# Performance work log

Hardware: AMD Instinct MI355X
Metric: run time of the kernel (lower is better)

Reference implementation:

```python
import jax, jax.numpy as jnp
import numpy as np

N_NODES = 50000
N_EDGES = 800000
IN_DIM = 256
HIDDEN = 64
HEADS1 = 4
HEADS2 = 1
N_CLASSES = 64
NEG_SLOPE = 0.2


def setup_inputs() -> dict:
    key = jax.random.key(0)
    ks = jax.random.split(key, 12)
    x = jax.random.normal(ks[0], (N_NODES, IN_DIM), dtype=jnp.float32)
    src = jax.random.randint(ks[1], (N_EDGES,), 0, N_NODES, dtype=jnp.int32)
    dst = jax.random.randint(ks[2], (N_EDGES,), 0, N_NODES, dtype=jnp.int32)
    s1 = 1.0 / np.sqrt(IN_DIM)
    s2 = 1.0 / np.sqrt(HIDDEN * HEADS1)
    W1 = jax.random.normal(ks[3], (IN_DIM, HEADS1 * HIDDEN), dtype=jnp.float32) * s1
    aL1 = jax.random.normal(ks[4], (HEADS1, HIDDEN), dtype=jnp.float32) * 0.1
    aR1 = jax.random.normal(ks[5], (HEADS1, HIDDEN), dtype=jnp.float32) * 0.1
    b1 = jnp.zeros((HEADS1 * HIDDEN,), dtype=jnp.float32)
    W2 = jax.random.normal(ks[6], (HEADS1 * HIDDEN, HEADS2 * N_CLASSES), dtype=jnp.float32) * s2
    aL2 = jax.random.normal(ks[7], (HEADS2, N_CLASSES), dtype=jnp.float32) * 0.1
    aR2 = jax.random.normal(ks[8], (HEADS2, N_CLASSES), dtype=jnp.float32) * 0.1
    b2 = jnp.zeros((HEADS2 * N_CLASSES,), dtype=jnp.float32)
    resW2 = jax.random.normal(ks[9], (HEADS1 * HIDDEN, HEADS2 * N_CLASSES), dtype=jnp.float32) * s2
    return {"x": x, "W1": W1, "aL1": aL1, "aR1": aR1, "b1": b1,
            "W2": W2, "aL2": aL2, "aR2": aR2, "b2": b2, "resW2": resW2,
            "src": src, "dst": dst}


def _gat_layer(h, W, aL, aR, b, src, dst, heads, out_dim, res_W=None, activation=None):
    n = h.shape[0]
    feat = (h @ W).reshape(n, heads, out_dim)          # [N, H, D]
    el = jnp.sum(feat * aL, axis=-1)                    # [N, H]
    er = jnp.sum(feat * aR, axis=-1)                    # [N, H]
    e = el[src] + er[dst]                               # [E, H]
    e = jnp.where(e > 0, e, NEG_SLOPE * e)              # leaky_relu
    # edge softmax over incoming edges of each destination node
    m = jax.ops.segment_max(e, dst, num_segments=n)
    ex = jnp.exp(e - m[dst])
    s = jax.ops.segment_sum(ex, dst, num_segments=n)
    sd = s[dst]
    a = ex / jnp.where(sd > 0, sd, 1.0)                 # [E, H]
    msg = feat[src] * a[:, :, None]                     # [E, H, D]
    rst = jax.ops.segment_sum(msg, dst, num_segments=n)  # [N, H, D]
    if res_W is not None:
        rst = rst + (h @ res_W).reshape(n, heads, out_dim)
    rst = rst + b.reshape(1, heads, out_dim)
    if activation is not None:
        rst = activation(rst)
    return rst


def reference(x, W1, aL1, aR1, b1, W2, aL2, aR2, b2, resW2, src, dst):
    h = _gat_layer(x, W1, aL1, aR1, b1, src, dst, HEADS1, HIDDEN,
                   res_W=None, activation=jax.nn.elu)
    h = h.reshape(N_NODES, HEADS1 * HIDDEN)             # flatten(1)
    h = _gat_layer(h, W2, aL2, aR2, b2, src, dst, HEADS2, N_CLASSES,
                   res_W=resW2, activation=None)
    return h.mean(axis=1)                               # mean over heads
```

## Files before the change

kernel.cpp:

```cpp
#include <hip/hip_runtime.h>
#include <hip/hip_bf16.h>
#include <math.h>

#define N_NODES 50000
#define N_EDGES 800000
#define IN_DIM  256
#define HID     64
#define H1      4
#define F1      256
#define NC      64
#define CHUNK   128
#define NB_SCAN 49
#define GEMM1_BLOCKS 800
#define FILL_BLOCKS  ((N_EDGES+255)/256)
#define HIST4_BLOCKS ((N_EDGES/4+255)/256)

typedef __attribute__((ext_vector_type(8))) short short8v;
typedef __attribute__((ext_vector_type(4))) float float4v;

__device__ __forceinline__ float bf2f(unsigned short u){
  union { unsigned int i; float f; } c; c.i = ((unsigned int)u) << 16; return c.f;
}


__global__ __launch_bounds__(256) void hist_prepw_kernel(
    const int* __restrict__ dst, int* __restrict__ counts,
    const float* __restrict__ W1, const float* __restrict__ W2,
    const float* __restrict__ resW2,
    __hip_bfloat16* __restrict__ W1T, __hip_bfloat16* __restrict__ B2T){
  int b = blockIdx.x;
  if (b < HIST4_BLOCKS){
    int e4 = b*256 + threadIdx.x;
    if (e4 < N_EDGES/4){
      int4 d = ((const int4*)dst)[e4];
      atomicAdd(&counts[d.x], 1);
      atomicAdd(&counts[d.y], 1);
      atomicAdd(&counts[d.z], 1);
      atomicAdd(&counts[d.w], 1);
    }
  } else {
    int i = (b - HIST4_BLOCKS)*256 + threadIdx.x;
    if (i < 256*256){
      int n = i >> 8, k = i & 255;
      W1T[n*256 + k] = __float2bfloat16(W1[k*256 + n]);
    } else if (i < 256*256 + 128*256){
      int j = i - 256*256;
      int n = j >> 8, k = j & 255;
      float v = (n < 64) ? W2[k*64 + n] : resW2[k*64 + (n - 64)];
      B2T[n*256 + k] = __float2bfloat16(v);
    }
  }
}


__global__ __launch_bounds__(1024) void scan1_kernel(const int* __restrict__ counts,
                                                     int* __restrict__ part,
                                                     int* __restrict__ bsum, int n){
  __shared__ int wsum[16];
  int b = blockIdx.x, tid = threadIdx.x;
  int i = b*1024 + tid;
  int lane = tid & 63, wid = tid >> 6;
  int x = (i < n) ? counts[i] : 0;
  #pragma unroll
  for (int off = 1; off < 64; off <<= 1){ int t = __shfl_up(x, off); if (lane >= off) x += t; }
  if (lane == 63) wsum[wid] = x;
  __syncthreads();
  if (wid == 0 && lane < 16){
    int w = wsum[lane];
    #pragma unroll
    for (int off = 1; off < 16; off <<= 1){ int t = __shfl_up(w, off); if (lane >= off) w += t; }
    wsum[lane] = w;
  }
  __syncthreads();
  int incl = x + (wid ? wsum[wid-1] : 0);
  if (i < n) part[i] = incl;
  if (tid == 1023) bsum[b] = incl;
}

__global__ __launch_bounds__(1024) void scan3_kernel(const int* __restrict__ part,
                                                     const int* __restrict__ bsum,
                                                     int* __restrict__ row_ptr,
                                                     int* __restrict__ cursor, int n){
  __shared__ int off_s;
  int b = blockIdx.x, tid = threadIdx.x;
  if (tid < 64){
    int orig = (tid < NB_SCAN) ? bsum[tid] : 0;
    int x = orig;
    #pragma unroll
    for (int o = 1; o < 64; o <<= 1){ int t = __shfl_up(x, o); if (tid >= o) x += t; }
    if (tid == b) off_s = x - orig;
  }
  __syncthreads();
  int i = b*1024 + tid;
  if (i < n){
    int v = part[i] + off_s;
    row_ptr[i+1] = v; cursor[i+1] = v;
  }
  if (i == 0){ row_ptr[0] = 0; cursor[0] = 0; }
}


template<int LAYER, bool AFP32>
__device__ __forceinline__ void gemm_body(
    const void* __restrict__ Araw,
    const __hip_bfloat16* __restrict__ BT,
    __hip_bfloat16* __restrict__ Fb,
    float* __restrict__ Res,
    float* __restrict__ el, float* __restrict__ er,
    const float* __restrict__ aL, const float* __restrict__ aR,
    int M, int bm, int bn)
{
  constexpr int K = 256;
  __shared__ __hip_bfloat16 As[128*72];
  __shared__ __hip_bfloat16 Bs[128*72];
  int tid = threadIdx.x;
  int lane = tid & 63, w = tid >> 6;
  int wr = w >> 1, wc = w & 1;
  int l15 = lane & 15, l4 = lane >> 4;

  float4v acc[4][4];
  #pragma unroll
  for (int i=0;i<4;i++)
    #pragma unroll
    for (int j=0;j<4;j++) acc[i][j] = (float4v){0.f,0.f,0.f,0.f};

  for (int kt = 0; kt < K; kt += 64){
    #pragma unroll
    for (int it = 0; it < 4; it++){
      int chunk = tid + it*256;
      int r = chunk >> 3, kc = (chunk & 7)*8;
      int arow = bm*128 + r;
      if (AFP32){
        const float* Af = (const float*)Araw;
        float4 v0 = make_float4(0,0,0,0), v1 = make_float4(0,0,0,0);
        if (arow < M){
          v0 = *(const float4*)&Af[(size_t)arow*K + kt + kc];
          v1 = *(const float4*)&Af[(size_t)arow*K + kt + kc + 4];
        }
        __hip_bfloat16 t[8] = {__float2bfloat16(v0.x),__float2bfloat16(v0.y),
                               __float2bfloat16(v0.z),__float2bfloat16(v0.w),
                               __float2bfloat16(v1.x),__float2bfloat16(v1.y),
                               __float2bfloat16(v1.z),__float2bfloat16(v1.w)};
        *(int4*)&As[r*72 + kc] = *(int4*)t;
      } else {
        const __hip_bfloat16* Ab = (const __hip_bfloat16*)Araw;
        int4 va = make_int4(0,0,0,0);
        if (arow < M) va = *(const int4*)&Ab[(size_t)arow*K + kt + kc];
        *(int4*)&As[r*72 + kc] = va;
      }
      int brow = bn*128 + r;
      int4 vb = *(const int4*)&BT[(size_t)brow*K + kt + kc];
      *(int4*)&Bs[r*72 + kc] = vb;
    }
    __syncthreads();
    short8v af[4][2], bfr[4][2];
    #pragma unroll
    for (int mi=0;mi<4;mi++)
      #pragma unroll
      for (int kf=0;kf<2;kf++)
        af[mi][kf] = *(const short8v*)&As[(wr*64 + mi*16 + l15)*72 + kf*32 + l4*8];
    #pragma unroll
    for (int ni=0;ni<4;ni++)
      #pragma unroll
      for (int kf=0;kf<2;kf++)
        bfr[ni][kf] = *(const short8v*)&Bs[(wc*64 + ni*16 + l15)*72 + kf*32 + l4*8];
    #pragma unroll
    for (int mi=0;mi<4;mi++)
      #pragma unroll
      for (int ni=0;ni<4;ni++){
        acc[mi][ni] = __builtin_amdgcn_mfma_f32_16x16x32_bf16(bfr[ni][0], af[mi][0], acc[mi][ni], 0,0,0);
        acc[mi][ni] = __builtin_amdgcn_mfma_f32_16x16x32_bf16(bfr[ni][1], af[mi][1], acc[mi][ni], 0,0,0);
      }
    __syncthreads();
  }

  if (LAYER == 1){
    int h = bn*2 + wc;
    float aLv[4][4], aRv[4][4];
    #pragma unroll
    for (int ni=0;ni<4;ni++){
      float4 a = *(const float4*)&aL[h*64 + ni*16 + l4*4];
      float4 bvv = *(const float4*)&aR[h*64 + ni*16 + l4*4];
      aLv[ni][0]=a.x; aLv[ni][1]=a.y; aLv[ni][2]=a.z; aLv[ni][3]=a.w;
      aRv[ni][0]=bvv.x; aRv[ni][1]=bvv.y; aRv[ni][2]=bvv.z; aRv[ni][3]=bvv.w;
    }
    #pragma unroll
    for (int mi=0;mi<4;mi++){
      int row = bm*128 + wr*64 + mi*16 + l15;
      float sl = 0.f, sr = 0.f;
      ushort4 packs[4];
      #pragma unroll
      for (int ni=0;ni<4;ni++){
        __hip_bfloat16 o[4];
        #pragma unroll
        for (int r=0;r<4;r++){
          float v = acc[mi][ni][r];
          sl += v*aLv[ni][r]; sr += v*aRv[ni][r];
          o[r] = __float2bfloat16(v);
        }
        packs[ni] = *(ushort4*)o;
      }
      if (row < M){
        #pragma unroll
        for (int ni=0;ni<4;ni++)
          *(ushort4*)&Fb[(size_t)row*256 + h*64 + ni*16 + l4*4] = packs[ni];
      }
      sl += __shfl_xor(sl, 16); sl += __shfl_xor(sl, 32);
      sr += __shfl_xor(sr, 16); sr += __shfl_xor(sr, 32);
      if (l4 == 0 && row < M){ el[row*4 + h] = sl; er[row*4 + h] = sr; }
    }
  } else {
    if (wc == 0){
      float aLv[4][4], aRv[4][4];
      #pragma unroll
      for (int ni=0;ni<4;ni++){
        float4 a = *(const float4*)&aL[ni*16 + l4*4];
        float4 bvv = *(const float4*)&aR[ni*16 + l4*4];
        aLv[ni][0]=a.x; aLv[ni][1]=a.y; aLv[ni][2]=a.z; aLv[ni][3]=a.w;
        aRv[ni][0]=bvv.x; aRv[ni][1]=bvv.y; aRv[ni][2]=bvv.z; aRv[ni][3]=bvv.w;
      }
      #pragma unroll
      for (int mi=0;mi<4;mi++){
        int row = bm*128 + wr*64 + mi*16 + l15;
        float sl = 0.f, sr = 0.f;
        ushort4 packs[4];
        #pragma unroll
        for (int ni=0;ni<4;ni++){
          __hip_bfloat16 o[4];
          #pragma unroll
          for (int r=0;r<4;r++){
            float v = acc[mi][ni][r];
            sl += v*aLv[ni][r]; sr += v*aRv[ni][r];
            o[r] = __float2bfloat16(v);
          }
          packs[ni] = *(ushort4*)o;
        }
        if (row < M){
          #pragma unroll
          for (int ni=0;ni<4;ni++)
            *(ushort4*)&Fb[(size_t)row*64 + ni*16 + l4*4] = packs[ni];
        }
        sl += __shfl_xor(sl, 16); sl += __shfl_xor(sl, 32);
        sr += __shfl_xor(sr, 16); sr += __shfl_xor(sr, 32);
        if (l4 == 0 && row < M){ el[row] = sl; er[row] = sr; }
      }
    } else {
      #pragma unroll
      for (int mi=0;mi<4;mi++){
        int row = bm*128 + wr*64 + mi*16 + l15;
        if (row < M){
          #pragma unroll
          for (int ni=0;ni<4;ni++){
            float4 o = make_float4(acc[mi][ni][0], acc[mi][ni][1], acc[mi][ni][2], acc[mi][ni][3]);
            *(float4*)&Res[(size_t)row*64 + ni*16 + l4*4] = o;
          }
        }
      }
    }
  }
}

__global__ __launch_bounds__(256) void gemm1_fill_kernel(
    const float* __restrict__ x, const __hip_bfloat16* __restrict__ W1T,
    __hip_bfloat16* __restrict__ featb,
    float* __restrict__ el, float* __restrict__ er,
    const float* __restrict__ aL, const float* __restrict__ aR,
    const int* __restrict__ src, const int* __restrict__ dst,
    int* __restrict__ cursor, int* __restrict__ csr_src)
{
  int id = blockIdx.x;
  if (id < GEMM1_BLOCKS){
    int bn = (id >> 3) & 1;
    int bm = (id & 7) | ((id >> 4) << 3);
    if (bm*128 >= N_NODES) return;
    gemm_body<1,true>(x, W1T, featb, nullptr, el, er, aL, aR, N_NODES, bm, bn);
  } else {
    int e = (id - GEMM1_BLOCKS)*256 + threadIdx.x;
    if (e < N_EDGES){
      int slot = atomicAdd(&cursor[dst[e]], 1);
      csr_src[slot] = src[e];
    }
  }
}

__global__ __launch_bounds__(256) void gemm2_kernel(
    const __hip_bfloat16* __restrict__ A, const __hip_bfloat16* __restrict__ BT,
    __hip_bfloat16* __restrict__ Fb, float* __restrict__ Res,
    float* __restrict__ el, float* __restrict__ er,
    const float* __restrict__ aL, const float* __restrict__ aR, int M)
{
  gemm_body<2,false>(A, BT, Fb, Res, el, er, aL, aR, M, blockIdx.x, 0);
}


__global__ __launch_bounds__(256) void agg1_kernel(const int* __restrict__ row_ptr,
                                                   const int* __restrict__ csr_src,
                                                   const float* __restrict__ el,
                                                   const float* __restrict__ er,
                                                   const __hip_bfloat16* __restrict__ featb,
                                                   const float* __restrict__ bias,
                                                   __hip_bfloat16* __restrict__ h1b, int N){
  __shared__ int   ssh[4][CHUNK];
  __shared__ float wsh[4][CHUNK][4];
  int b = blockIdx.x;
  int slot = b & 7, ch = slot >> 2, sub = slot & 3, g = b >> 3;
  int lane = threadIdx.x & 63, wv = threadIdx.x >> 6;
  int n = g*16 + sub*4 + wv;
  if (n >= N) return;
  int rs = row_ptr[n], re = row_ptr[n+1];
  int half = lane >> 5;
  int l31 = lane & 31;
  int c0 = ch*128 + l31*4;
  int hl = c0 >> 6;
  float4 ern4 = *(const float4*)&er[(size_t)n*4];
  float ernv[4] = {ern4.x, ern4.y, ern4.z, ern4.w};
  float acc[4] = {0.f,0.f,0.f,0.f};
  float ssum4[4] = {0.f,0.f,0.f,0.f};

  for (int base = rs; base < re; base += CHUNK){
    int cnt = min(CHUNK, re - base);
    int padded = (cnt + 7) & ~7;
    for (int t = lane; t < padded; t += 64){
      float w4[4] = {0.f,0.f,0.f,0.f};
      int s = 0;
      if (t < cnt){
        s = csr_src[base + t];
        float4 e4 = *(const float4*)&el[(size_t)s*4];
        float ev[4] = {e4.x, e4.y, e4.z, e4.w};
        #pragma unroll
        for (int h = 0; h < 4; h++){
          float e = ev[h] + ernv[h];
          e = e > 0.f ? e : 0.2f*e;
          float ex = __expf(e);
          w4[h] = ex;
          ssum4[h] += ex;
        }
      }
      ssh[wv][t] = s;
      *(float4*)&wsh[wv][t][0] = make_float4(w4[0], w4[1], w4[2], w4[3]);
    }
    for (int jb = 0; jb < padded; jb += 8){
      int t0 = jb + half, t1 = jb + 2 + half, t2 = jb + 4 + half, t3 = jb + 6 + half;
      int s0 = ssh[wv][t0], s1 = ssh[wv][t1], s2 = ssh[wv][t2], s3 = ssh[wv][t3];
      float w0 = wsh[wv][t0][hl], w1 = wsh[wv][t1][hl];
      float w2 = wsh[wv][t2][hl], w3 = wsh[wv][t3][hl];
      ushort4 f0 = *(const ushort4*)&featb[(size_t)s0*256 + c0];
      ushort4 f1 = *(const ushort4*)&featb[(size_t)s1*256 + c0];
      ushort4 f2 = *(const ushort4*)&featb[(size_t)s2*256 + c0];
      ushort4 f3 = *(const ushort4*)&featb[(size_t)s3*256 + c0];
      acc[0] += w0*bf2f(f0.x) + w1*bf2f(f1.x) + w2*bf2f(f2.x) + w3*bf2f(f3.x);
      acc[1] += w0*bf2f(f0.y) + w1*bf2f(f1.y) + w2*bf2f(f2.y) + w3*bf2f(f3.y);
      acc[2] += w0*bf2f(f0.z) + w1*bf2f(f1.z) + w2*bf2f(f2.z) + w3*bf2f(f3.z);
      acc[3] += w0*bf2f(f0.w) + w1*bf2f(f1.w) + w2*bf2f(f2.w) + w3*bf2f(f3.w);
    }
  }
  #pragma unroll
  for (int off = 32; off; off >>= 1)
    #pragma unroll
    for (int h = 0; h < 4; h++) ssum4[h] += __shfl_xor(ssum4[h], off);
  #pragma unroll
  for (int q = 0; q < 4; q++) acc[q] += __shfl_xor(acc[q], 32);
  float inv = ssum4[hl] > 0.f ? 1.f/ssum4[hl] : 0.f;
  if (lane < 32){
    float4 b4 = *(const float4*)&bias[c0];
    float bb[4] = {b4.x, b4.y, b4.z, b4.w};
    __hip_bfloat16 o[4];
    #pragma unroll
    for (int q = 0; q < 4; q++){
      float v = acc[q]*inv + bb[q];
      v = v > 0.f ? v : __expf(v) - 1.f;
      o[q] = __float2bfloat16(v);
    }
    *(ushort4*)&h1b[(size_t)n*256 + c0] = *(ushort4*)o;
  }
}

__global__ __launch_bounds__(256) void agg2_kernel(const int* __restrict__ row_ptr,
                                                   const int* __restrict__ csr_src,
                                                   const float* __restrict__ el,
                                                   const float* __restrict__ er,
                                                   const __hip_bfloat16* __restrict__ f2b,
                                                   const float* __restrict__ res,
                                                   const float* __restrict__ bias,
                                                   float* __restrict__ out, int N){
  __shared__ int   ssh[4][CHUNK];
  __shared__ float wsh[4][CHUNK];
  int lane = threadIdx.x & 63, wv = threadIdx.x >> 6;
  int n = blockIdx.x*4 + wv;
  if (n >= N) return;
  int rs = row_ptr[n], re = row_ptr[n+1];
  int q4 = lane >> 4;
  int l15 = lane & 15;
  float ern = er[n];
  float acc[4] = {0.f,0.f,0.f,0.f};
  float ssum = 0.f;

  for (int base = rs; base < re; base += CHUNK){
    int cnt = min(CHUNK, re - base);
    int padded = (cnt + 15) & ~15;
    for (int t = lane; t < padded; t += 64){
      float w = 0.f; int s = 0;
      if (t < cnt){
        s = csr_src[base + t];
        float e = el[s] + ern;
        e = e > 0.f ? e : 0.2f*e;
        w = __expf(e);
        ssum += w;
      }
      ssh[wv][t] = s;
      wsh[wv][t] = w;
    }
    for (int jb = 0; jb < padded; jb += 16){
      int t0 = jb + q4, t1 = jb + 4 + q4, t2 = jb + 8 + q4, t3 = jb + 12 + q4;
      int s0 = ssh[wv][t0], s1 = ssh[wv][t1], s2 = ssh[wv][t2], s3 = ssh[wv][t3];
      float w0 = wsh[wv][t0], w1 = wsh[wv][t1], w2 = wsh[wv][t2], w3 = wsh[wv][t3];
      ushort4 f0 = *(const ushort4*)&f2b[(size_t)s0*NC + l15*4];
      ushort4 f1 = *(const ushort4*)&f2b[(size_t)s1*NC + l15*4];
      ushort4 f2 = *(const ushort4*)&f2b[(size_t)s2*NC + l15*4];
      ushort4 f3 = *(const ushort4*)&f2b[(size_t)s3*NC + l15*4];
      acc[0] += w0*bf2f(f0.x) + w1*bf2f(f1.x) + w2*bf2f(f2.x) + w3*bf2f(f3.x);
      acc[1] += w0*bf2f(f0.y) + w1*bf2f(f1.y) + w2*bf2f(f2.y) + w3*bf2f(f3.y);
      acc[2] += w0*bf2f(f0.z) + w1*bf2f(f1.z) + w2*bf2f(f2.z) + w3*bf2f(f3.z);
      acc[3] += w0*bf2f(f0.w) + w1*bf2f(f1.w) + w2*bf2f(f2.w) + w3*bf2f(f3.w);
    }
  }
  #pragma unroll
  for (int off = 32; off; off >>= 1) ssum += __shfl_xor(ssum, off);
  #pragma unroll
  for (int q = 0; q < 4; q++){
    acc[q] += __shfl_xor(acc[q], 16);
    acc[q] += __shfl_xor(acc[q], 32);
  }
  float inv = ssum > 0.f ? 1.f/ssum : 0.f;
  if (lane < 16){
    float4 r4 = *(const float4*)&res[(size_t)n*NC + l15*4];
    float4 b4 = *(const float4*)&bias[l15*4];
    float4 o;
    o.x = acc[0]*inv + r4.x + b4.x;
    o.y = acc[1]*inv + r4.y + b4.y;
    o.z = acc[2]*inv + r4.z + b4.z;
    o.w = acc[3]*inv + r4.w + b4.w;
    *(float4*)&out[(size_t)n*NC + l15*4] = o;
  }
}


extern "C" void kernel_launch(void* const* d_in, const int* in_sizes, int n_in,
                              void* d_out, int out_size, void* d_ws, size_t ws_size,
                              hipStream_t stream){
  const float* x     = (const float*)d_in[0];
  const float* W1    = (const float*)d_in[1];
  const float* aL1   = (const float*)d_in[2];
  const float* aR1   = (const float*)d_in[3];
  const float* b1    = (const float*)d_in[4];
  const float* W2    = (const float*)d_in[5];
  const float* aL2   = (const float*)d_in[6];
  const float* aR2   = (const float*)d_in[7];
  const float* b2    = (const float*)d_in[8];
  const float* resW2 = (const float*)d_in[9];
  const int*   src   = (const int*)d_in[10];
  const int*   dst   = (const int*)d_in[11];
  float* out = (float*)d_out;

  char* p = (char*)d_ws;
  auto alloc = [&](size_t bytes)->void*{
    void* r = (void*)p; p += (bytes + 255) & ~(size_t)255; return r;
  };
  __hip_bfloat16* featb = (__hip_bfloat16*)alloc((size_t)N_NODES*F1*2);
  __hip_bfloat16* h1b   = (__hip_bfloat16*)alloc((size_t)N_NODES*F1*2);
  __hip_bfloat16* f2b   = (__hip_bfloat16*)alloc((size_t)N_NODES*NC*2);
  float* res   = (float*)alloc((size_t)N_NODES*NC*4);
  float* el1   = (float*)alloc((size_t)N_NODES*H1*4);
  float* er1   = (float*)alloc((size_t)N_NODES*H1*4);
  float* el2   = (float*)alloc((size_t)N_NODES*4);
  float* er2   = (float*)alloc((size_t)N_NODES*4);
  int* counts  = (int*)alloc((size_t)N_NODES*4);
  int* part    = (int*)alloc((size_t)N_NODES*4);
  int* bsum    = (int*)alloc((size_t)64*4);
  int* row_ptr = (int*)alloc((size_t)(N_NODES+1)*4);
  int* cursor  = (int*)alloc((size_t)(N_NODES+1)*4);
  int* csr_src = (int*)alloc((size_t)N_EDGES*4);
  __hip_bfloat16* W1T = (__hip_bfloat16*)alloc((size_t)256*256*2);
  __hip_bfloat16* B2T = (__hip_bfloat16*)alloc((size_t)128*256*2);

  int nb = (N_NODES + 1023)/1024;
  int prepw_blocks = (256*256 + 128*256 + 255)/256;
  hipMemsetAsync(counts, 0, (size_t)N_NODES*4, stream);
  hist_prepw_kernel<<<HIST4_BLOCKS + prepw_blocks, 256, 0, stream>>>(dst, counts,
                                                                     W1, W2, resW2, W1T, B2T);
  scan1_kernel<<<nb, 1024, 0, stream>>>(counts, part, bsum, N_NODES);
  scan3_kernel<<<nb, 1024, 0, stream>>>(part, bsum, row_ptr, cursor, N_NODES);

  gemm1_fill_kernel<<<GEMM1_BLOCKS + FILL_BLOCKS, 256, 0, stream>>>(
      x, W1T, featb, el1, er1, aL1, aR1, src, dst, cursor, csr_src);

  agg1_kernel<<<25000, 256, 0, stream>>>(row_ptr, csr_src, el1, er1, featb, b1, h1b, N_NODES);

  gemm2_kernel<<<(N_NODES+127)/128, 256, 0, stream>>>(h1b, B2T, f2b, res,
                                                      el2, er2, aL2, aR2, N_NODES);
  agg2_kernel<<<(N_NODES+3)/4, 256, 0, stream>>>(row_ptr, csr_src, el2, er2, f2b, res, b2, out, N_NODES);
}
```

Baseline: 212.7 us.

## Process full 256-wide feature row per wave in layer-1 aggregation with 16-byte loads

The layer-1 aggregation kernel previously split each node's 256 channels across two blocks (128 channels each), so every node recomputed its edge softmax weights twice. Now one wave covers all 256 channels using 8-element bf16 vector loads per lane and unrolls over 8 edges per iteration, halving the block count. This removes the duplicated edge-weight computation and index loads and widens the global loads. The cost is higher register pressure from 8 accumulators and 8 in-flight vector loads, plus more padding per chunk (multiples of 16).

```diff
diff --git a/kernel.cpp b/kernel.cpp
--- a/kernel.cpp
+++ b/kernel.cpp
@@ -302,24 +302,21 @@
                                                    __hip_bfloat16* __restrict__ h1b, int N){
   __shared__ int   ssh[4][CHUNK];
   __shared__ float wsh[4][CHUNK][4];
-  int b = blockIdx.x;
-  int slot = b & 7, ch = slot >> 2, sub = slot & 3, g = b >> 3;
   int lane = threadIdx.x & 63, wv = threadIdx.x >> 6;
-  int n = g*16 + sub*4 + wv;
+  int n = blockIdx.x*4 + wv;
   if (n >= N) return;
   int rs = row_ptr[n], re = row_ptr[n+1];
   int half = lane >> 5;
   int l31 = lane & 31;
-  int c0 = ch*128 + l31*4;
-  int hl = c0 >> 6;
+  int hl = l31 >> 3;
   float4 ern4 = *(const float4*)&er[(size_t)n*4];
   float ernv[4] = {ern4.x, ern4.y, ern4.z, ern4.w};
-  float acc[4] = {0.f,0.f,0.f,0.f};
+  float acc[8] = {0.f,0.f,0.f,0.f,0.f,0.f,0.f,0.f};
   float ssum4[4] = {0.f,0.f,0.f,0.f};
 
   for (int base = rs; base < re; base += CHUNK){
     int cnt = min(CHUNK, re - base);
-    int padded = (cnt + 7) & ~7;
+    int padded = (cnt + 15) & ~15;
     for (int t = lane; t < padded; t += 64){
       float w4[4] = {0.f,0.f,0.f,0.f};
       int s = 0;
@@ -339,19 +336,34 @@
       ssh[wv][t] = s;
       *(float4*)&wsh[wv][t][0] = make_float4(w4[0], w4[1], w4[2], w4[3]);
     }
-    for (int jb = 0; jb < padded; jb += 8){
-      int t0 = jb + half, t1 = jb + 2 + half, t2 = jb + 4 + half, t3 = jb + 6 + half;
-      int s0 = ssh[wv][t0], s1 = ssh[wv][t1], s2 = ssh[wv][t2], s3 = ssh[wv][t3];
-      float w0 = wsh[wv][t0][hl], w1 = wsh[wv][t1][hl];
-      float w2 = wsh[wv][t2][hl], w3 = wsh[wv][t3][hl];
-      ushort4 f0 = *(const ushort4*)&featb[(size_t)s0*256 + c0];
-      ushort4 f1 = *(const ushort4*)&featb[(size_t)s1*256 + c0];
-      ushort4 f2 = *(const ushort4*)&featb[(size_t)s2*256 + c0];
-      ushort4 f3 = *(const ushort4*)&featb[(size_t)s3*256 + c0];
-      acc[0] += w0*bf2f(f0.x) + w1*bf2f(f1.x) + w2*bf2f(f2.x) + w3*bf2f(f3.x);
-      acc[1] += w0*bf2f(f0.y) + w1*bf2f(f1.y) + w2*bf2f(f2.y) + w3*bf2f(f3.y);
-      acc[2] += w0*bf2f(f0.z) + w1*bf2f(f1.z) + w2*bf2f(f2.z) + w3*bf2f(f3.z);
-      acc[3] += w0*bf2f(f0.w) + w1*bf2f(f1.w) + w2*bf2f(f2.w) + w3*bf2f(f3.w);
+    for (int jb = 0; jb < padded; jb += 16){
+      int s0 = ssh[wv][jb +      half], s1 = ssh[wv][jb +  2 + half];
+      int s2 = ssh[wv][jb +  4 + half], s3 = ssh[wv][jb +  6 + half];
+      int s4 = ssh[wv][jb +  8 + half], s5 = ssh[wv][jb + 10 + half];
+      int s6 = ssh[wv][jb + 12 + half], s7 = ssh[wv][jb + 14 + half];
+      float w0 = wsh[wv][jb +      half][hl], w1 = wsh[wv][jb +  2 + half][hl];
+      float w2 = wsh[wv][jb +  4 + half][hl], w3 = wsh[wv][jb +  6 + half][hl];
+      float w4_ = wsh[wv][jb +  8 + half][hl], w5 = wsh[wv][jb + 10 + half][hl];
+      float w6 = wsh[wv][jb + 12 + half][hl], w7 = wsh[wv][jb + 14 + half][hl];
+      short8v f0 = *(const short8v*)&featb[(size_t)s0*256 + l31*8];
+      short8v f1 = *(const short8v*)&featb[(size_t)s1*256 + l31*8];
+      short8v f2 = *(const short8v*)&featb[(size_t)s2*256 + l31*8];
+      short8v f3 = *(const short8v*)&featb[(size_t)s3*256 + l31*8];
+      short8v f4 = *(const short8v*)&featb[(size_t)s4*256 + l31*8];
+      short8v f5 = *(const short8v*)&featb[(size_t)s5*256 + l31*8];
+      short8v f6 = *(const short8v*)&featb[(size_t)s6*256 + l31*8];
+      short8v f7 = *(const short8v*)&featb[(size_t)s7*256 + l31*8];
+      #pragma unroll
+      for (int q = 0; q < 8; q++){
+        acc[q] += w0 * bf2f((unsigned short)f0[q]);
+        acc[q] += w1 * bf2f((unsigned short)f1[q]);
+        acc[q] += w2 * bf2f((unsigned short)f2[q]);
+        acc[q] += w3 * bf2f((unsigned short)f3[q]);
+        acc[q] += w4_ * bf2f((unsigned short)f4[q]);
+        acc[q] += w5 * bf2f((unsigned short)f5[q]);
+        acc[q] += w6 * bf2f((unsigned short)f6[q]);
+        acc[q] += w7 * bf2f((unsigned short)f7[q]);
+      }
     }
   }
   #pragma unroll
@@ -359,19 +371,20 @@
     #pragma unroll
     for (int h = 0; h < 4; h++) ssum4[h] += __shfl_xor(ssum4[h], off);
   #pragma unroll
-  for (int q = 0; q < 4; q++) acc[q] += __shfl_xor(acc[q], 32);
+  for (int q = 0; q < 8; q++) acc[q] += __shfl_xor(acc[q], 32);
   float inv = ssum4[hl] > 0.f ? 1.f/ssum4[hl] : 0.f;
   if (lane < 32){
-    float4 b4 = *(const float4*)&bias[c0];
-    float bb[4] = {b4.x, b4.y, b4.z, b4.w};
-    __hip_bfloat16 o[4];
-    #pragma unroll
-    for (int q = 0; q < 4; q++){
+    float4 b0 = *(const float4*)&bias[l31*8];
+    float4 b1v = *(const float4*)&bias[l31*8 + 4];
+    float bb[8] = {b0.x,b0.y,b0.z,b0.w,b1v.x,b1v.y,b1v.z,b1v.w};
+    __hip_bfloat16 o[8];
+    #pragma unroll
+    for (int q = 0; q < 8; q++){
       float v = acc[q]*inv + bb[q];
       v = v > 0.f ? v : __expf(v) - 1.f;
       o[q] = __float2bfloat16(v);
     }
-    *(ushort4*)&h1b[(size_t)n*256 + c0] = *(ushort4*)o;
+    *(short8v*)&h1b[(size_t)n*256 + l31*8] = *(short8v*)o;
   }
 }
 
@@ -494,7 +507,7 @@
   gemm1_fill_kernel<<<GEMM1_BLOCKS + FILL_BLOCKS, 256, 0, stream>>>(
       x, W1T, featb, el1, er1, aL1, aR1, src, dst, cursor, csr_src);
 
-  agg1_kernel<<<25000, 256, 0, stream>>>(row_ptr, csr_src, el1, er1, featb, b1, h1b, N_NODES);
+  agg1_kernel<<<(N_NODES+3)/4, 256, 0, stream>>>(row_ptr, csr_src, el1, er1, featb, b1, h1b, N_NODES);
 
   gemm2_kernel<<<(N_NODES+127)/128, 256, 0, stream>>>(h1b, B2T, f2b, res,
                                                       el2, er2, aL2, aR2, N_NODES);
```

Result: slower. 222.1 us (+4.4%).
